# Kernel optimization log

Hardware: AMD Instinct MI355X
Metric: run time of the kernel (lower is better)

The kernel has to match this reference:

```python
import jax, jax.numpy as jnp
import numpy as np

B, N, D, M = 16, 8192, 512, 1024


def setup_inputs() -> dict:
    key = jax.random.key(0)
    k1, k2 = jax.random.split(key)
    x = jax.random.normal(k1, (B, N, D), dtype=jnp.float32)
    mem = jax.random.normal(k2, (1, D, M), dtype=jnp.float32)  # learned memory bank
    return {"x": x, "mem": mem}


def reference(x, mem):
    # forward_mem: memory-slot cross-attention
    # x: [B, N, D]; mem: [1, D, M] (broadcast over batch)
    d = x.shape[-1]
    m = mem[0]  # [D, M]
    # logits[b, m, n] = sum_d mem[d, m] * x[b, n, d] / sqrt(D)  -> [B, M, N]
    logits = jnp.einsum('dm,bnd->bmn', m, x) / jnp.sqrt(jnp.asarray(d, x.dtype))
    # softmax over the memory-slot axis (dim=1 in torch == axis 1 here)
    attn = jax.nn.softmax(logits, axis=1)  # [B, M, N]
    # x_new[b, n, d] = sum_m mem[d, m] * attn[b, m, n]
    out = jnp.einsum('dm,bmn->bnd', m, attn)  # [B, N, D]
    return out
```

## Files before the change

kernel.cpp:

```cpp
#include <hip/hip_runtime.h>

#define B_ 16
#define N_ 8192
#define D_ 512
#define M_ 1024
#define BT 64
#define SCALE 0.04419417382415922f

typedef __attribute__((ext_vector_type(8))) short short8;
typedef __attribute__((ext_vector_type(4))) short short4v;
typedef __attribute__((ext_vector_type(4))) float f32x4;
typedef __attribute__((ext_vector_type(16))) float f32x16;

__device__ __forceinline__ unsigned short f2bf(float f) {
  unsigned int u = __float_as_uint(f);
  u += 0x7FFFu + ((u >> 16) & 1u);
  return (unsigned short)(u >> 16);
}
__device__ __forceinline__ float bf2f(unsigned short h) {
  return __uint_as_float(((unsigned int)h) << 16);
}

#define MFMA32(a, b, c) __builtin_amdgcn_mfma_f32_32x32x16_bf16((a), (b), (c), 0, 0, 0)

__global__ void prep_mem_kernel(const float* __restrict__ mem,
                                unsigned short* __restrict__ memTbF,
                                unsigned short* __restrict__ memDF) {
  int t = blockIdx.x * 256 + threadIdx.x;
  int j = t & 7, l = (t >> 3) & 63, blk = t >> 9;
  {
    int kk = blk & 31, MT = blk >> 5;
    int m = MT * 32 + (l & 31);
    int d = kk * 16 + ((l >> 5) << 3) + j;
    memTbF[t] = f2bf(mem[d * M_ + m] * SCALE);
  }
  {
    int kg = blk & 63, DT = blk >> 6;
    int d = DT * 32 + (l & 31);
    int m = kg * 16 + ((l >> 5) << 3) + j;
    memDF[t] = f2bf(mem[d * M_ + m]);
  }
}

__global__ __launch_bounds__(256, 2) void fused_kernel(
    const float* __restrict__ x, const unsigned short* __restrict__ memTbF,
    const unsigned short* __restrict__ memDF, float* __restrict__ out) {
  __shared__ unsigned short sX[32768];
  __shared__ unsigned short sPa[8192];
  float* psums = (float*)sX;
  float* sInv = ((float*)sX) + 256;

  const int tid = threadIdx.x;
  const int w = tid >> 6;
  const int lane = tid & 63;
  const int c31 = lane & 31;
  const int l5 = lane >> 5;
  const int e7 = lane & 7;
  const int t15 = c31 & 15;
  const long t0 = (long)blockIdx.x * BT;

  {
    const int row = tid >> 2, cg = tid & 3;
    const int r7 = row & 7;
    const float* xp = x + (t0 + row) * (long)D_ + cg * 128;
    char* sxb = (char*)sX + (row << 10);
#pragma unroll
    for (int j = 0; j < 16; j++) {
      f32x4 v0 = *(const f32x4*)(xp + j * 8);
      f32x4 v1 = *(const f32x4*)(xp + j * 8 + 4);
      short8 o;
      o[0] = (short)f2bf(v0[0]);
      o[1] = (short)f2bf(v0[1]);
      o[2] = (short)f2bf(v0[2]);
      o[3] = (short)f2bf(v0[3]);
      o[4] = (short)f2bf(v1[0]);
      o[5] = (short)f2bf(v1[1]);
      o[6] = (short)f2bf(v1[2]);
      o[7] = (short)f2bf(v1[3]);
      int s = (cg << 4) + j;
      *(short8*)(sxb + ((s ^ r7) << 4)) = o;
    }
  }
  __syncthreads();

  f32x16 oacc[2][4];
#pragma unroll
  for (int tt = 0; tt < 2; tt++)
#pragma unroll
    for (int d0 = 0; d0 < 4; d0++) oacc[tt][d0] = (f32x16)0.0f;
  f32x16 sacc[2];
  float fsum[2] = {0.f, 0.f};

  char* const bx0 = (char*)sX + (c31 << 10);
  char* const bx1 = (char*)sX + ((32 + c31) << 10);
  char* const bp0 = (char*)sPa + (c31 << 8);
  char* const bp1 = (char*)sPa + ((32 + c31) << 8);

  auto gemm1 = [&](int ch) {
    sacc[0] = (f32x16)0.0f;
    sacc[1] = (f32x16)0.0f;
    const short8* ga = (const short8*)memTbF + (size_t)((ch * 4 + w) * 32) * 64 + lane;
#pragma unroll
    for (int kk = 0; kk < 32; kk++) {
      short8 a = ga[kk * 64];
      int sw = (((kk << 1) | l5) ^ e7) << 4;
      short8 x0 = *(const short8*)(bx0 + sw);
      short8 x1 = *(const short8*)(bx1 + sw);
      sacc[0] = MFMA32(a, x0, sacc[0]);
      sacc[1] = MFMA32(a, x1, sacc[1]);
    }
  };

  auto pgen = [&]() {
#pragma unroll
    for (int tt = 0; tt < 2; tt++) {
      int tok = tt * 32 + c31;
      char* base = (char*)sPa + (tok << 8);
      float s = 0.f;
      unsigned short pb[16];
#pragma unroll
      for (int q = 0; q < 16; q++) {
        float p = __expf(sacc[tt][q]);
        unsigned short b = f2bf(p);
        pb[q] = b;
        s += bf2f(b);
      }
      fsum[tt] += s;
#pragma unroll
      for (int q = 0; q < 4; q++) {
        short4v o = {(short)pb[q * 4], (short)pb[q * 4 + 1],
                     (short)pb[q * 4 + 2], (short)pb[q * 4 + 3]};
        int sl = ((w << 2) | q) ^ t15;
        *(short4v*)(base + (sl << 4) + (l5 << 3)) = o;
      }
    }
  };

  gemm1(0);
  pgen();

#pragma unroll 1
  for (int c = 0; c < 8; c++) {
    __syncthreads();
    if (c == 7 && tid < BT) {
      float s = psums[tid] + psums[64 + tid] + psums[128 + tid] + psums[192 + tid];
      sInv[tid] = 1.0f / s;
    }
    {
      const short8* gb = (const short8*)memDF + ((size_t)(w * 4) * 64 + c * 8) * 64 + lane;
      const bool doG1 = (c < 7);
      const short8* ga = (const short8*)memTbF +
                         (size_t)((((c + 1) & 7) * 4 + w) * 32) * 64 + lane;
      if (doG1) {
        sacc[0] = (f32x16)0.0f;
        sacc[1] = (f32x16)0.0f;
      }
#pragma unroll
      for (int k0 = 0; k0 < 8; k0++) {
        int sp = ((((k0 << 1) | l5) ^ t15) << 4);
        short8 p0 = *(const short8*)(bp0 + sp);
        short8 p1 = *(const short8*)(bp1 + sp);
        short8 b0 = gb[(0 * 64 + k0) * 64];
        short8 b1 = gb[(1 * 64 + k0) * 64];
        short8 b2 = gb[(2 * 64 + k0) * 64];
        short8 b3 = gb[(3 * 64 + k0) * 64];
        oacc[0][0] = MFMA32(p0, b0, oacc[0][0]);
        oacc[1][0] = MFMA32(p1, b0, oacc[1][0]);
        oacc[0][1] = MFMA32(p0, b1, oacc[0][1]);
        oacc[1][1] = MFMA32(p1, b1, oacc[1][1]);
        oacc[0][2] = MFMA32(p0, b2, oacc[0][2]);
        oacc[1][2] = MFMA32(p1, b2, oacc[1][2]);
        oacc[0][3] = MFMA32(p0, b3, oacc[0][3]);
        oacc[1][3] = MFMA32(p1, b3, oacc[1][3]);
        if (doG1) {
#pragma unroll
          for (int kq = 0; kq < 4; kq++) {
            int kk = k0 * 4 + kq;
            short8 a = ga[kk * 64];
            int sw = (((kk << 1) | l5) ^ e7) << 4;
            short8 x0 = *(const short8*)(bx0 + sw);
            short8 x1 = *(const short8*)(bx1 + sw);
            sacc[0] = MFMA32(a, x0, sacc[0]);
            sacc[1] = MFMA32(a, x1, sacc[1]);
          }
        }
      }
    }
    __syncthreads();
    if (c < 7) {
      pgen();
      if (c == 6) {
        float s0 = fsum[0] + __shfl_xor(fsum[0], 32);
        float s1 = fsum[1] + __shfl_xor(fsum[1], 32);
        if (lane < 32) {
          psums[w * 64 + lane] = s0;
          psums[w * 64 + 32 + lane] = s1;
        }
      }
    }
  }

#pragma unroll
  for (int tt = 0; tt < 2; tt++) {
#pragma unroll
    for (int q = 0; q < 16; q++) {
      int tok = tt * 32 + (q & 3) + ((q >> 2) << 3) + (l5 << 2);
      float inv = sInv[tok];
      float* op = out + (t0 + tok) * (long)D_ + w * 128 + c31;
#pragma unroll
      for (int d0 = 0; d0 < 4; d0++) op[d0 * 32] = oacc[tt][d0][q] * inv;
    }
  }
}

extern "C" void kernel_launch(void* const* d_in, const int* in_sizes, int n_in,
                              void* d_out, int out_size, void* d_ws, size_t ws_size,
                              hipStream_t stream) {
  const float* x = (const float*)d_in[0];
  const float* mem = (const float*)d_in[1];
  float* out = (float*)d_out;
  unsigned short* memTbF = (unsigned short*)d_ws;
  unsigned short* memDF = memTbF + (size_t)D_ * M_;

  hipLaunchKernelGGL(prep_mem_kernel, dim3((D_ * M_) / 256), dim3(256), 0, stream,
                     mem, memTbF, memDF);
  hipLaunchKernelGGL(fused_kernel, dim3((B_ * N_) / BT), dim3(256), 0, stream,
                     x, memTbF, memDF, out);
}
```

Before: 452.2 us.

## Split fused attention block across eight waves and fold softmax row-sum into GEMM2

Doubles the workgroup to 512 threads. The first GEMM is split over four memory-slot wave groups and two token halves, and the second GEMM is split over eight waves that each own 64 output columns, so each wave holds fewer accumulators. The softmax denominator is no longer accumulated in pgen through a cross-wave psums reduction. Instead, two waves sum the bf16 probabilities they already read during the second GEMM. The aim is more resident waves per CU to hide latency, at the cost of more threads per block contending for the same LDS and barriers.

```diff
diff --git a/kernel.cpp b/kernel.cpp
--- a/kernel.cpp
+++ b/kernel.cpp
@@ -42,13 +42,11 @@
   }
 }
 
-__global__ __launch_bounds__(256, 2) void fused_kernel(
+__global__ __launch_bounds__(512, 4) void fused_kernel(
     const float* __restrict__ x, const unsigned short* __restrict__ memTbF,
     const unsigned short* __restrict__ memDF, float* __restrict__ out) {
   __shared__ unsigned short sX[32768];
   __shared__ unsigned short sPa[8192];
-  float* psums = (float*)sX;
-  float* sInv = ((float*)sX) + 256;
 
   const int tid = threadIdx.x;
   const int w = tid >> 6;
@@ -56,18 +54,22 @@
   const int c31 = lane & 31;
   const int l5 = lane >> 5;
   const int e7 = lane & 7;
-  const int t15 = c31 & 15;
+  const int t15 = lane & 15;
+  const int mslot = w & 3;
+  const int tslot = w >> 2;
   const long t0 = (long)blockIdx.x * BT;
 
   {
-    const int row = tid >> 2, cg = tid & 3;
+    const int row = tid >> 3;
+    const int cslot = tid & 7;
     const int r7 = row & 7;
-    const float* xp = x + (t0 + row) * (long)D_ + cg * 128;
+    const float* xp = x + (t0 + row) * (long)D_;
     char* sxb = (char*)sX + (row << 10);
 #pragma unroll
-    for (int j = 0; j < 16; j++) {
-      f32x4 v0 = *(const f32x4*)(xp + j * 8);
-      f32x4 v1 = *(const f32x4*)(xp + j * 8 + 4);
+    for (int j = 0; j < 8; j++) {
+      const int s = cslot + 8 * j;
+      f32x4 v0 = *(const f32x4*)(xp + s * 8);
+      f32x4 v1 = *(const f32x4*)(xp + s * 8 + 4);
       short8 o;
       o[0] = (short)f2bf(v0[0]);
       o[1] = (short)f2bf(v0[1]);
@@ -77,62 +79,45 @@
       o[5] = (short)f2bf(v1[1]);
       o[6] = (short)f2bf(v1[2]);
       o[7] = (short)f2bf(v1[3]);
-      int s = (cg << 4) + j;
       *(short8*)(sxb + ((s ^ r7) << 4)) = o;
     }
   }
   __syncthreads();
 
-  f32x16 oacc[2][4];
+  f32x16 oacc[2][2];
 #pragma unroll
   for (int tt = 0; tt < 2; tt++)
 #pragma unroll
-    for (int d0 = 0; d0 < 4; d0++) oacc[tt][d0] = (f32x16)0.0f;
-  f32x16 sacc[2];
-  float fsum[2] = {0.f, 0.f};
-
-  char* const bx0 = (char*)sX + (c31 << 10);
-  char* const bx1 = (char*)sX + ((32 + c31) << 10);
+    for (int d0 = 0; d0 < 2; d0++) oacc[tt][d0] = (f32x16)0.0f;
+  f32x16 sacc;
+  float dsum = 0.f;
+
+  char* const bx = (char*)sX + ((tslot * 32 + c31) << 10);
   char* const bp0 = (char*)sPa + (c31 << 8);
   char* const bp1 = (char*)sPa + ((32 + c31) << 8);
+  char* const bpw = (char*)sPa + ((tslot * 32 + c31) << 8);
 
   auto gemm1 = [&](int ch) {
-    sacc[0] = (f32x16)0.0f;
-    sacc[1] = (f32x16)0.0f;
-    const short8* ga = (const short8*)memTbF + (size_t)((ch * 4 + w) * 32) * 64 + lane;
+    sacc = (f32x16)0.0f;
+    const short8* ga =
+        (const short8*)memTbF + (size_t)((ch * 4 + mslot) * 32) * 64 + lane;
 #pragma unroll
     for (int kk = 0; kk < 32; kk++) {
       short8 a = ga[kk * 64];
       int sw = (((kk << 1) | l5) ^ e7) << 4;
-      short8 x0 = *(const short8*)(bx0 + sw);
-      short8 x1 = *(const short8*)(bx1 + sw);
-      sacc[0] = MFMA32(a, x0, sacc[0]);
-      sacc[1] = MFMA32(a, x1, sacc[1]);
+      short8 xv = *(const short8*)(bx + sw);
+      sacc = MFMA32(a, xv, sacc);
     }
   };
 
   auto pgen = [&]() {
 #pragma unroll
-    for (int tt = 0; tt < 2; tt++) {
-      int tok = tt * 32 + c31;
-      char* base = (char*)sPa + (tok << 8);
-      float s = 0.f;
-      unsigned short pb[16];
-#pragma unroll
-      for (int q = 0; q < 16; q++) {
-        float p = __expf(sacc[tt][q]);
-        unsigned short b = f2bf(p);
-        pb[q] = b;
-        s += bf2f(b);
-      }
-      fsum[tt] += s;
-#pragma unroll
-      for (int q = 0; q < 4; q++) {
-        short4v o = {(short)pb[q * 4], (short)pb[q * 4 + 1],
-                     (short)pb[q * 4 + 2], (short)pb[q * 4 + 3]};
-        int sl = ((w << 2) | q) ^ t15;
-        *(short4v*)(base + (sl << 4) + (l5 << 3)) = o;
-      }
+    for (int h = 0; h < 4; h++) {
+      short4v o;
+#pragma unroll
+      for (int i = 0; i < 4; i++) o[i] = (short)f2bf(__expf(sacc[h * 4 + i]));
+      int sl = ((mslot << 2) | h) ^ t15;
+      *(short4v*)(bpw + (sl << 4) + (l5 << 3)) = o;
     }
   };
 
@@ -142,73 +127,68 @@
 #pragma unroll 1
   for (int c = 0; c < 8; c++) {
     __syncthreads();
-    if (c == 7 && tid < BT) {
-      float s = psums[tid] + psums[64 + tid] + psums[128 + tid] + psums[192 + tid];
-      sInv[tid] = 1.0f / s;
-    }
     {
-      const short8* gb = (const short8*)memDF + ((size_t)(w * 4) * 64 + c * 8) * 64 + lane;
+      const short8* gb0 =
+          (const short8*)memDF + (size_t)((w * 2 + 0) * 64 + c * 8) * 64 + lane;
+      const short8* gb1 =
+          (const short8*)memDF + (size_t)((w * 2 + 1) * 64 + c * 8) * 64 + lane;
       const bool doG1 = (c < 7);
       const short8* ga = (const short8*)memTbF +
-                         (size_t)((((c + 1) & 7) * 4 + w) * 32) * 64 + lane;
-      if (doG1) {
-        sacc[0] = (f32x16)0.0f;
-        sacc[1] = (f32x16)0.0f;
-      }
+                         (size_t)(((c + 1) * 4 + mslot) * 32) * 64 + lane;
+      if (doG1) sacc = (f32x16)0.0f;
 #pragma unroll
       for (int k0 = 0; k0 < 8; k0++) {
-        int sp = ((((k0 << 1) | l5) ^ t15) << 4);
+        int sp = (((k0 << 1) | l5) ^ t15) << 4;
         short8 p0 = *(const short8*)(bp0 + sp);
         short8 p1 = *(const short8*)(bp1 + sp);
-        short8 b0 = gb[(0 * 64 + k0) * 64];
-        short8 b1 = gb[(1 * 64 + k0) * 64];
-        short8 b2 = gb[(2 * 64 + k0) * 64];
-        short8 b3 = gb[(3 * 64 + k0) * 64];
+        short8 b0 = gb0[k0 * 64];
+        short8 b1 = gb1[k0 * 64];
         oacc[0][0] = MFMA32(p0, b0, oacc[0][0]);
         oacc[1][0] = MFMA32(p1, b0, oacc[1][0]);
         oacc[0][1] = MFMA32(p0, b1, oacc[0][1]);
         oacc[1][1] = MFMA32(p1, b1, oacc[1][1]);
-        oacc[0][2] = MFMA32(p0, b2, oacc[0][2]);
-        oacc[1][2] = MFMA32(p1, b2, oacc[1][2]);
-        oacc[0][3] = MFMA32(p0, b3, oacc[0][3]);
-        oacc[1][3] = MFMA32(p1, b3, oacc[1][3]);
+        if (w == 0) {
+#pragma unroll
+          for (int e = 0; e < 8; e++) dsum += bf2f((unsigned short)p0[e]);
+        } else if (w == 1) {
+#pragma unroll
+          for (int e = 0; e < 8; e++) dsum += bf2f((unsigned short)p1[e]);
+        }
         if (doG1) {
 #pragma unroll
           for (int kq = 0; kq < 4; kq++) {
             int kk = k0 * 4 + kq;
             short8 a = ga[kk * 64];
             int sw = (((kk << 1) | l5) ^ e7) << 4;
-            short8 x0 = *(const short8*)(bx0 + sw);
-            short8 x1 = *(const short8*)(bx1 + sw);
-            sacc[0] = MFMA32(a, x0, sacc[0]);
-            sacc[1] = MFMA32(a, x1, sacc[1]);
+            short8 xv = *(const short8*)(bx + sw);
+            sacc = MFMA32(a, xv, sacc);
           }
         }
       }
     }
     __syncthreads();
-    if (c < 7) {
-      pgen();
-      if (c == 6) {
-        float s0 = fsum[0] + __shfl_xor(fsum[0], 32);
-        float s1 = fsum[1] + __shfl_xor(fsum[1], 32);
-        if (lane < 32) {
-          psums[w * 64 + lane] = s0;
-          psums[w * 64 + 32 + lane] = s1;
-        }
-      }
-    }
-  }
+    if (c < 7) pgen();
+  }
+
+  float* sInvF = (float*)sPa;
+  if (w == 0) {
+    float s = dsum + __shfl_xor(dsum, 32);
+    if (lane < 32) sInvF[lane] = 1.0f / s;
+  } else if (w == 1) {
+    float s = dsum + __shfl_xor(dsum, 32);
+    if (lane < 32) sInvF[32 + lane] = 1.0f / s;
+  }
+  __syncthreads();
 
 #pragma unroll
   for (int tt = 0; tt < 2; tt++) {
 #pragma unroll
     for (int q = 0; q < 16; q++) {
-      int tok = tt * 32 + (q & 3) + ((q >> 2) << 3) + (l5 << 2);
-      float inv = sInv[tok];
-      float* op = out + (t0 + tok) * (long)D_ + w * 128 + c31;
-#pragma unroll
-      for (int d0 = 0; d0 < 4; d0++) op[d0 * 32] = oacc[tt][d0][q] * inv;
+      int token = tt * 32 + (q & 3) + ((q >> 2) << 3) + (l5 << 2);
+      float inv = sInvF[token];
+      float* op = out + (t0 + token) * (long)D_ + w * 64 + c31;
+      op[0] = oacc[tt][0][q] * inv;
+      op[32] = oacc[tt][1][q] * inv;
     }
   }
 }
@@ -224,6 +204,6 @@
 
   hipLaunchKernelGGL(prep_mem_kernel, dim3((D_ * M_) / 256), dim3(256), 0, stream,
                      mem, memTbF, memDF);
-  hipLaunchKernelGGL(fused_kernel, dim3((B_ * N_) / BT), dim3(256), 0, stream,
+  hipLaunchKernelGGL(fused_kernel, dim3((B_ * N_) / BT), dim3(512), 0, stream,
                      x, memTbF, memDF, out);
 }
```

After: 539.6 us. 19.3% more time.

## Split fused attention into separate GEMM1+exp and GEMM2 kernels via global P

Applied to the files above, without the earlier changes.

The single fused kernel, which interleaved the logits GEMM, exp and the output GEMM through shared memory with per-chunk barriers, is split into two kernels. The first kernel writes unnormalised bf16 probabilities in the MFMA fragment layout straight from registers, using the output buffer as scratch, plus per-token inverse denominators. The second kernel streams those fragments and memory-bank fragments from global memory into the output GEMM. memDF is re-laid out so the stored P register layout can be used directly as the MFMA operand. The aim is to remove LDS round-trips and block-wide syncs from the fused loop, at the cost of an extra ~256MB write and read of P through HBM.

```diff
diff --git a/kernel.cpp b/kernel.cpp
--- a/kernel.cpp
+++ b/kernel.cpp
@@ -8,7 +8,6 @@
 #define SCALE 0.04419417382415922f
 
 typedef __attribute__((ext_vector_type(8))) short short8;
-typedef __attribute__((ext_vector_type(4))) short short4v;
 typedef __attribute__((ext_vector_type(4))) float f32x4;
 typedef __attribute__((ext_vector_type(16))) float f32x16;
 
@@ -37,18 +36,17 @@
   {
     int kg = blk & 63, DT = blk >> 6;
     int d = DT * 32 + (l & 31);
-    int m = kg * 16 + ((l >> 5) << 3) + j;
+    int hi = l >> 5;
+    int m = (kg >> 1) * 32 + ((kg & 1) << 4) + (hi << 2) + (j & 3) + ((j >> 2) << 3);
     memDF[t] = f2bf(mem[d * M_ + m]);
   }
 }
 
-__global__ __launch_bounds__(256, 2) void fused_kernel(
+__global__ __launch_bounds__(256, 2) void gemm1_exp_kernel(
     const float* __restrict__ x, const unsigned short* __restrict__ memTbF,
-    const unsigned short* __restrict__ memDF, float* __restrict__ out) {
+    unsigned short* __restrict__ Pf, float* __restrict__ denomInv) {
   __shared__ unsigned short sX[32768];
-  __shared__ unsigned short sPa[8192];
-  float* psums = (float*)sX;
-  float* sInv = ((float*)sX) + 256;
+  __shared__ float psums[4][64];
 
   const int tid = threadIdx.x;
   const int w = tid >> 6;
@@ -56,7 +54,6 @@
   const int c31 = lane & 31;
   const int l5 = lane >> 5;
   const int e7 = lane & 7;
-  const int t15 = c31 & 15;
   const long t0 = (long)blockIdx.x * BT;
 
   {
@@ -83,122 +80,110 @@
   }
   __syncthreads();
 
-  f32x16 oacc[2][4];
-#pragma unroll
-  for (int tt = 0; tt < 2; tt++)
-#pragma unroll
-    for (int d0 = 0; d0 < 4; d0++) oacc[tt][d0] = (f32x16)0.0f;
-  f32x16 sacc[2];
-  float fsum[2] = {0.f, 0.f};
-
   char* const bx0 = (char*)sX + (c31 << 10);
   char* const bx1 = (char*)sX + ((32 + c31) << 10);
-  char* const bp0 = (char*)sPa + (c31 << 8);
-  char* const bp1 = (char*)sPa + ((32 + c31) << 8);
-
-  auto gemm1 = [&](int ch) {
-    sacc[0] = (f32x16)0.0f;
-    sacc[1] = (f32x16)0.0f;
-    const short8* ga = (const short8*)memTbF + (size_t)((ch * 4 + w) * 32) * 64 + lane;
-#pragma unroll
+  short8* const Pf8 = (short8*)Pf;
+  float fsum0 = 0.f, fsum1 = 0.f;
+
+  auto emit = [&](f32x16 sv, int tt, int mtile) {
+    unsigned short pb[16];
+    float s = 0.f;
+#pragma unroll
+    for (int q = 0; q < 16; q++) {
+      float p = __expf(sv[q]);
+      unsigned short b = f2bf(p);
+      pb[q] = b;
+      s += bf2f(b);
+    }
+    if (tt == 0) fsum0 += s; else fsum1 += s;
+    size_t TTg = (size_t)blockIdx.x * 2 + tt;
+#pragma unroll
+    for (int sb = 0; sb < 2; sb++) {
+      short8 o;
+#pragma unroll
+      for (int e = 0; e < 8; e++) o[e] = (short)pb[sb * 8 + e];
+      Pf8[(TTg * 64 + (size_t)(mtile * 2 + sb)) * 64 + lane] = o;
+    }
+  };
+
+#pragma unroll 1
+  for (int i = 0; i < 4; i++) {
+    const int mt0 = i * 8 + w * 2;
+    f32x16 s00 = (f32x16)0.0f, s01 = (f32x16)0.0f;
+    f32x16 s10 = (f32x16)0.0f, s11 = (f32x16)0.0f;
+    const short8* ga0 = (const short8*)memTbF + (size_t)(mt0 * 32) * 64 + lane;
+    const short8* ga1 = ga0 + 32 * 64;
+#pragma unroll 8
     for (int kk = 0; kk < 32; kk++) {
-      short8 a = ga[kk * 64];
+      short8 a0 = ga0[kk * 64];
+      short8 a1 = ga1[kk * 64];
       int sw = (((kk << 1) | l5) ^ e7) << 4;
       short8 x0 = *(const short8*)(bx0 + sw);
       short8 x1 = *(const short8*)(bx1 + sw);
-      sacc[0] = MFMA32(a, x0, sacc[0]);
-      sacc[1] = MFMA32(a, x1, sacc[1]);
-    }
-  };
-
-  auto pgen = [&]() {
-#pragma unroll
-    for (int tt = 0; tt < 2; tt++) {
-      int tok = tt * 32 + c31;
-      char* base = (char*)sPa + (tok << 8);
-      float s = 0.f;
-      unsigned short pb[16];
-#pragma unroll
-      for (int q = 0; q < 16; q++) {
-        float p = __expf(sacc[tt][q]);
-        unsigned short b = f2bf(p);
-        pb[q] = b;
-        s += bf2f(b);
-      }
-      fsum[tt] += s;
-#pragma unroll
-      for (int q = 0; q < 4; q++) {
-        short4v o = {(short)pb[q * 4], (short)pb[q * 4 + 1],
-                     (short)pb[q * 4 + 2], (short)pb[q * 4 + 3]};
-        int sl = ((w << 2) | q) ^ t15;
-        *(short4v*)(base + (sl << 4) + (l5 << 3)) = o;
-      }
-    }
-  };
-
-  gemm1(0);
-  pgen();
-
-#pragma unroll 1
-  for (int c = 0; c < 8; c++) {
-    __syncthreads();
-    if (c == 7 && tid < BT) {
-      float s = psums[tid] + psums[64 + tid] + psums[128 + tid] + psums[192 + tid];
-      sInv[tid] = 1.0f / s;
-    }
-    {
-      const short8* gb = (const short8*)memDF + ((size_t)(w * 4) * 64 + c * 8) * 64 + lane;
-      const bool doG1 = (c < 7);
-      const short8* ga = (const short8*)memTbF +
-                         (size_t)((((c + 1) & 7) * 4 + w) * 32) * 64 + lane;
-      if (doG1) {
-        sacc[0] = (f32x16)0.0f;
-        sacc[1] = (f32x16)0.0f;
-      }
-#pragma unroll
-      for (int k0 = 0; k0 < 8; k0++) {
-        int sp = ((((k0 << 1) | l5) ^ t15) << 4);
-        short8 p0 = *(const short8*)(bp0 + sp);
-        short8 p1 = *(const short8*)(bp1 + sp);
-        short8 b0 = gb[(0 * 64 + k0) * 64];
-        short8 b1 = gb[(1 * 64 + k0) * 64];
-        short8 b2 = gb[(2 * 64 + k0) * 64];
-        short8 b3 = gb[(3 * 64 + k0) * 64];
-        oacc[0][0] = MFMA32(p0, b0, oacc[0][0]);
-        oacc[1][0] = MFMA32(p1, b0, oacc[1][0]);
-        oacc[0][1] = MFMA32(p0, b1, oacc[0][1]);
-        oacc[1][1] = MFMA32(p1, b1, oacc[1][1]);
-        oacc[0][2] = MFMA32(p0, b2, oacc[0][2]);
-        oacc[1][2] = MFMA32(p1, b2, oacc[1][2]);
-        oacc[0][3] = MFMA32(p0, b3, oacc[0][3]);
-        oacc[1][3] = MFMA32(p1, b3, oacc[1][3]);
-        if (doG1) {
-#pragma unroll
-          for (int kq = 0; kq < 4; kq++) {
-            int kk = k0 * 4 + kq;
-            short8 a = ga[kk * 64];
-            int sw = (((kk << 1) | l5) ^ e7) << 4;
-            short8 x0 = *(const short8*)(bx0 + sw);
-            short8 x1 = *(const short8*)(bx1 + sw);
-            sacc[0] = MFMA32(a, x0, sacc[0]);
-            sacc[1] = MFMA32(a, x1, sacc[1]);
-          }
-        }
-      }
-    }
-    __syncthreads();
-    if (c < 7) {
-      pgen();
-      if (c == 6) {
-        float s0 = fsum[0] + __shfl_xor(fsum[0], 32);
-        float s1 = fsum[1] + __shfl_xor(fsum[1], 32);
-        if (lane < 32) {
-          psums[w * 64 + lane] = s0;
-          psums[w * 64 + 32 + lane] = s1;
-        }
-      }
-    }
-  }
+      s00 = MFMA32(a0, x0, s00);
+      s01 = MFMA32(a0, x1, s01);
+      s10 = MFMA32(a1, x0, s10);
+      s11 = MFMA32(a1, x1, s11);
+    }
+    emit(s00, 0, mt0);
+    emit(s01, 1, mt0);
+    emit(s10, 0, mt0 + 1);
+    emit(s11, 1, mt0 + 1);
+  }
+
+  fsum0 += __shfl_xor(fsum0, 32);
+  fsum1 += __shfl_xor(fsum1, 32);
+  if (l5 == 0) {
+    psums[w][c31] = fsum0;
+    psums[w][32 + c31] = fsum1;
+  }
+  __syncthreads();
+  if (tid < 64)
+    denomInv[t0 + tid] =
+        1.0f / (psums[0][tid] + psums[1][tid] + psums[2][tid] + psums[3][tid]);
+}
+
+__global__ __launch_bounds__(256, 2) void gemm2_kernel(
+    const unsigned short* __restrict__ Pf, const unsigned short* __restrict__ memDF,
+    const float* __restrict__ denomInv, float* __restrict__ out) {
+  __shared__ float sInv[64];
+  const int tid = threadIdx.x;
+  const int w = tid >> 6;
+  const int lane = tid & 63;
+  const int c31 = lane & 31;
+  const int l5 = lane >> 5;
+  const long t0 = (long)blockIdx.x * BT;
+  if (tid < 64) sInv[tid] = denomInv[t0 + tid];
+
+  f32x16 oacc[2][4];
+#pragma unroll
+  for (int tt = 0; tt < 2; tt++)
+#pragma unroll
+    for (int d0 = 0; d0 < 4; d0++) oacc[tt][d0] = (f32x16)0.0f;
+
+  const short8* pa0 = (const short8*)Pf + ((size_t)blockIdx.x * 2) * 4096 + lane;
+  const short8* pa1 = pa0 + 4096;
+  const short8* gb = (const short8*)memDF + (size_t)(w * 4) * 4096 + lane;
+
+#pragma unroll 4
+  for (int kg = 0; kg < 64; kg++) {
+    short8 p0 = pa0[kg * 64];
+    short8 p1 = pa1[kg * 64];
+    short8 b0 = gb[(0 * 64 + kg) * 64];
+    short8 b1 = gb[(1 * 64 + kg) * 64];
+    short8 b2 = gb[(2 * 64 + kg) * 64];
+    short8 b3 = gb[(3 * 64 + kg) * 64];
+    oacc[0][0] = MFMA32(p0, b0, oacc[0][0]);
+    oacc[1][0] = MFMA32(p1, b0, oacc[1][0]);
+    oacc[0][1] = MFMA32(p0, b1, oacc[0][1]);
+    oacc[1][1] = MFMA32(p1, b1, oacc[1][1]);
+    oacc[0][2] = MFMA32(p0, b2, oacc[0][2]);
+    oacc[1][2] = MFMA32(p1, b2, oacc[1][2]);
+    oacc[0][3] = MFMA32(p0, b3, oacc[0][3]);
+    oacc[1][3] = MFMA32(p1, b3, oacc[1][3]);
+  }
+
+  __syncthreads();
 
 #pragma unroll
   for (int tt = 0; tt < 2; tt++) {
@@ -221,9 +206,13 @@
   float* out = (float*)d_out;
   unsigned short* memTbF = (unsigned short*)d_ws;
   unsigned short* memDF = memTbF + (size_t)D_ * M_;
+  float* denomInv = (float*)(memDF + (size_t)D_ * M_);
+  unsigned short* Pf = (unsigned short*)d_out;
 
   hipLaunchKernelGGL(prep_mem_kernel, dim3((D_ * M_) / 256), dim3(256), 0, stream,
                      mem, memTbF, memDF);
-  hipLaunchKernelGGL(fused_kernel, dim3((B_ * N_) / BT), dim3(256), 0, stream,
-                     x, memTbF, memDF, out);
-}
+  hipLaunchKernelGGL(gemm1_exp_kernel, dim3((B_ * N_) / BT), dim3(256), 0, stream,
+                     x, memTbF, Pf, denomInv);
+  hipLaunchKernelGGL(gemm2_kernel, dim3((B_ * N_) / BT), dim3(256), 0, stream,
+                     Pf, memDF, denomInv, out);
+}
```

Result: slower. 507.6 us (+12.3%).
